# Kernel optimization log

Hardware: AMD Instinct MI355X
Metric: run time of the kernel (lower is better)

The kernel has to match this reference:

```python
import math
import jax, jax.numpy as jnp
import numpy as np

B, N_COLS, CHANNELS, NUM_HEADS = 512, 128, 512, 8
D_HEAD = CHANNELS // NUM_HEADS


def setup_inputs() -> dict:
    key = jax.random.key(0)
    ks = jax.random.split(key, 9)
    s = 1.0 / math.sqrt(CHANNELS)
    x = jax.random.normal(ks[0], (B, N_COLS, CHANNELS), dtype=jnp.float32)
    Wq = jax.random.uniform(ks[1], (CHANNELS, CHANNELS), jnp.float32, -s, s)
    bq = jax.random.uniform(ks[2], (CHANNELS,), jnp.float32, -s, s)
    Wk = jax.random.uniform(ks[3], (CHANNELS, CHANNELS), jnp.float32, -s, s)
    bk = jax.random.uniform(ks[4], (CHANNELS,), jnp.float32, -s, s)
    Wv = jax.random.uniform(ks[5], (CHANNELS, CHANNELS), jnp.float32, -s, s)
    bv = jax.random.uniform(ks[6], (CHANNELS,), jnp.float32, -s, s)
    Wo = jax.random.uniform(ks[7], (CHANNELS, CHANNELS), jnp.float32, -s, s)
    bo = jax.random.uniform(ks[8], (CHANNELS,), jnp.float32, -s, s)
    return {"x": x, "Wq": Wq, "bq": bq, "Wk": Wk, "bk": bk,
            "Wv": Wv, "bv": bv, "Wo": Wo, "bo": bo}


def reference(x, Wq, bq, Wk, bk, Wv, bv, Wo, bo):
    b, n, c = x.shape
    h, d = NUM_HEADS, D_HEAD

    def split_heads(t):  # [b, n, c] -> [b, h, n, d]
        return t.reshape(b, n, h, d).transpose(0, 2, 1, 3)

    Q = split_heads(x @ Wq + bq)
    K = split_heads(x @ Wk + bk)
    V = split_heads(x @ Wv + bv)

    # raw scores [b, h, q, k]
    scores = jnp.einsum('bhqd,bhkd->bhqk', Q, K)
    # causal mask over columns; note: mask added BEFORE scaling by sqrt(d)
    causal = jnp.tril(jnp.ones((n, n), dtype=jnp.float32))
    mask = (1.0 - causal) * -100000.0
    attn = jax.nn.softmax((scores + mask) / math.sqrt(d), axis=-1)
    out = jnp.einsum('bhqk,bhkd->bhqd', attn, V)
    out = out.transpose(0, 2, 1, 3).reshape(b, n, c)
    return out @ Wo + bo
```

## Files before the change

kernel.cpp:

```cpp
#include <hip/hip_runtime.h>

typedef _Float16 f16;
typedef _Float16 half8 __attribute__((ext_vector_type(8)));
typedef _Float16 half4 __attribute__((ext_vector_type(4)));
typedef float f32x4 __attribute__((ext_vector_type(4)));

#define B_SZ 512
#define NQ   128
#define CH   512
#define NH   8
#define DH   64
#define MTOK (B_SZ*NQ)
#define KD   512

#define MFMA16(a,b,c) __builtin_amdgcn_mfma_f32_16x16x32_f16((a),(b),(c),0,0,0)

#define GLDS16(g,l) __builtin_amdgcn_global_load_lds( \
    (__attribute__((address_space(1))) void*)(g), \
    (__attribute__((address_space(3))) void*)(l), 16, 0, 0)

__global__ __launch_bounds__(256) void k_cvt(const float* __restrict__ x,
                                             f16* __restrict__ xb) {
  const int n8 = MTOK * KD / 8;
  int i = blockIdx.x * blockDim.x + threadIdx.x;
  const int stride = gridDim.x * blockDim.x;
  for (; i < n8; i += stride) {
    f32x4 a = ((const f32x4*)x)[2 * i];
    f32x4 b = ((const f32x4*)x)[2 * i + 1];
    half8 h;
    h[0] = (f16)a[0]; h[1] = (f16)a[1]; h[2] = (f16)a[2]; h[3] = (f16)a[3];
    h[4] = (f16)b[0]; h[5] = (f16)b[1]; h[6] = (f16)b[2]; h[7] = (f16)b[3];
    ((half8*)xb)[i] = h;
  }
}

__global__ __launch_bounds__(256) void k_wt(const float* __restrict__ Wq,
                                            const float* __restrict__ Wk,
                                            const float* __restrict__ Wv,
                                            const float* __restrict__ Wo,
                                            f16* __restrict__ wt) {
  const int n = blockIdx.x;
  const float* W = (n < 512) ? Wq : (n < 1024) ? Wk : (n < 1536) ? Wv : Wo;
  const int c = n & 511;
  for (int k = threadIdx.x; k < 512; k += blockDim.x)
    wt[n * 512 + k] = (f16)W[k * 512 + c];
}


template<bool SW, int MB>
__device__ __forceinline__ void mfma16x(f32x4 (&acc)[8][4], half8 (&af)[4], half8 (&bf)[4]) {
#pragma unroll
  for (int i = 0; i < 4; ++i)
#pragma unroll
    for (int n = 0; n < 4; ++n) {
      if (SW) acc[MB + i][n] = MFMA16(bf[n], af[i], acc[MB + i][n]);
      else    acc[MB + i][n] = MFMA16(af[i], bf[n], acc[MB + i][n]);
    }
}

__device__ __forceinline__ void load4(const f16* base, half8 (&fr)[4]) {
#pragma unroll
  for (int n = 0; n < 4; ++n) fr[n] = *(const half8*)(base + n * 512);
}

#define BAR_MFMA_OPEN() __builtin_amdgcn_s_barrier(); \
  asm volatile("s_waitcnt lgkmcnt(0)" ::: "memory"); \
  __builtin_amdgcn_sched_barrier(0); \
  __builtin_amdgcn_s_setprio(1)
#define MFMA_CLOSE() __builtin_amdgcn_s_setprio(0); __builtin_amdgcn_s_barrier()
#define MFMA_CLOSE_GATE4() __builtin_amdgcn_s_setprio(0); \
  asm volatile("s_waitcnt vmcnt(4)" ::: "memory"); \
  __builtin_amdgcn_s_barrier()
#define MFMA_CLOSE_GATE0() __builtin_amdgcn_s_setprio(0); \
  asm volatile("s_waitcnt vmcnt(0)" ::: "memory"); \
  __builtin_amdgcn_s_barrier()

template<bool SW>
__device__ __forceinline__ void gemm256_main(
    const f16* __restrict__ Ag, const f16* __restrict__ Bg,
    int arow0, f16* lds, f32x4 (&acc)[8][4]) {
  const int tid = threadIdx.x;
  const int w = tid >> 6, lane = tid & 63;
  const int ln = lane & 15, g = lane >> 4;
  const int wm = w >> 2, wn = w & 3;
  const int slotx = ((g ^ ((ln >> 1) & 3)) << 3);

  f16* la = lds;
  f16* lb = lds + 32768;

  const int gsrc = (((tid & 3) ^ ((tid >> 3) & 3)) << 3);
  int soA[4], soB[4];
#pragma unroll
  for (int ks2 = 0; ks2 < 2; ++ks2)
#pragma unroll
    for (int r = 0; r < 2; ++r) {
      soA[ks2 * 2 + r] = (arow0 + r * 128 + (tid >> 2)) * KD + ks2 * 32 + gsrc;
      soB[ks2 * 2 + r] = (r * 128 + (tid >> 2)) * KD + ks2 * 32 + gsrc;
    }
  const int ldst = w * 512;

#define STAGE_A(t, ks2, r) GLDS16((f16*)Ag + soA[(ks2)*2+(r)] + (t)*64, \
      la + ((t)&1)*16384 + (ks2)*8192 + (r)*4096 + ldst)
#define STAGE_B(t, ks2, r) GLDS16((f16*)Bg + soB[(ks2)*2+(r)] + (t)*64, \
      lb + ((t)&1)*16384 + (ks2)*8192 + (r)*4096 + ldst)

  const int raA = (wm * 128 + ln) * 32 + slotx;
  const int raB = (wn * 64 + ln) * 32 + slotx;

  STAGE_A(0, 0, 0); STAGE_A(0, 0, 1); STAGE_B(0, 0, 0); STAGE_B(0, 0, 1);
  STAGE_A(0, 1, 0); STAGE_A(0, 1, 1); STAGE_B(0, 1, 0); STAGE_B(0, 1, 1);
  asm volatile("s_waitcnt vmcnt(0)" ::: "memory");
  __builtin_amdgcn_s_barrier();

  half8 af[4], bf[4];

#pragma unroll 1
  for (int t = 0; t < 7; ++t) {
    const int cur = t & 1;
    const f16* lac = la + cur * 16384;
    const f16* lbc = lb + cur * 16384;
    load4(lbc + raB, bf);
    load4(lac + raA, af);
    STAGE_A(t + 1, 0, 0); STAGE_A(t + 1, 0, 1);
    BAR_MFMA_OPEN(); mfma16x<SW, 0>(acc, af, bf); MFMA_CLOSE();
    load4(lac + raA + 4 * 512, af);
    STAGE_B(t + 1, 0, 0); STAGE_B(t + 1, 0, 1);
    BAR_MFMA_OPEN(); mfma16x<SW, 4>(acc, af, bf); MFMA_CLOSE_GATE4();
    load4(lbc + 8192 + raB, bf);
    load4(lac + 8192 + raA, af);
    STAGE_A(t + 1, 1, 0); STAGE_A(t + 1, 1, 1);
    BAR_MFMA_OPEN(); mfma16x<SW, 0>(acc, af, bf); MFMA_CLOSE();
    load4(lac + 8192 + raA + 4 * 512, af);
    STAGE_B(t + 1, 1, 0); STAGE_B(t + 1, 1, 1);
    BAR_MFMA_OPEN(); mfma16x<SW, 4>(acc, af, bf); MFMA_CLOSE_GATE4();
  }
  {
    const f16* lac = la + 16384;
    const f16* lbc = lb + 16384;
    load4(lbc + raB, bf);
    load4(lac + raA, af);
    BAR_MFMA_OPEN(); mfma16x<SW, 0>(acc, af, bf); MFMA_CLOSE();
    load4(lac + raA + 4 * 512, af);
    BAR_MFMA_OPEN(); mfma16x<SW, 4>(acc, af, bf); MFMA_CLOSE_GATE0();
    load4(lbc + 8192 + raB, bf);
    load4(lac + 8192 + raA, af);
    BAR_MFMA_OPEN(); mfma16x<SW, 0>(acc, af, bf); MFMA_CLOSE();
    load4(lac + 8192 + raA + 4 * 512, af);
    __builtin_amdgcn_s_barrier();
    asm volatile("s_waitcnt lgkmcnt(0)" ::: "memory");
    __builtin_amdgcn_sched_barrier(0);
    mfma16x<SW, 4>(acc, af, bf);
  }
#undef STAGE_A
#undef STAGE_B
}

__global__ __launch_bounds__(512, 2) void k_qk256(
    const f16* __restrict__ A, const f16* __restrict__ wt,
    const float* __restrict__ bq, const float* __restrict__ bk,
    f16* __restrict__ qb, f16* __restrict__ kb) {
  __shared__ f16 smem[65536];
  const int nwg8 = 1024 / 8;
  const int f = (blockIdx.x & 7) * nwg8 + (blockIdx.x >> 3);
  const int ntile = f & 3, mtile = f >> 2;
  const int arow0 = mtile * 256;
  const f16* Bg = wt + ntile * 256 * KD;

  f32x4 acc[8][4] = {};
  gemm256_main<true>(A, Bg, arow0, smem, acc);

  const int tid = threadIdx.x;
  const int w = tid >> 6, lane = tid & 63;
  const int ln = lane & 15, g = lane >> 4;
  const int wm = w >> 2, wn = w & 3;
  const int cslab = (ntile & 1) << 8;
  const float* bias = (ntile < 2) ? bq : bk;
  f16* dst = (ntile < 2) ? qb : kb;
#pragma unroll
  for (int n = 0; n < 4; ++n) {
    const int cg = cslab + wn * 64 + n * 16 + g * 4;
    const f32x4 b4 = *(const f32x4*)(bias + cg);
    const int h = cg >> 6, d = cg & 63;
#pragma unroll
    for (int m = 0; m < 8; ++m) {
      const int tk = arow0 + wm * 128 + m * 16 + ln;
      const int b = tk >> 7, tr = tk & 127;
      half4 o;
#pragma unroll
      for (int r = 0; r < 4; ++r) o[r] = (f16)(acc[m][n][r] + b4[r]);
      *(half4*)(dst + ((b * NH + h) * NQ + tr) * DH + d) = o;
    }
  }
}

__global__ __launch_bounds__(512, 2) void k_v256(
    const f16* __restrict__ A, const f16* __restrict__ wt,
    const float* __restrict__ bv, f16* __restrict__ vb) {
  __shared__ f16 smem[65536];
  const int nwg8 = 512 / 8;
  const int f = (blockIdx.x & 7) * nwg8 + (blockIdx.x >> 3);
  const int ntile = f & 1, mtile = f >> 1;
  const int arow0 = mtile * 256;
  const f16* Bg = wt + (1024 + ntile * 256) * KD;

  f32x4 acc[8][4] = {};
  gemm256_main<false>(A, Bg, arow0, smem, acc);

  const int tid = threadIdx.x;
  const int w = tid >> 6, lane = tid & 63;
  const int ln = lane & 15, g = lane >> 4;
  const int wm = w >> 2, wn = w & 3;
#pragma unroll
  for (int n = 0; n < 4; ++n) {
    const int cg = ntile * 256 + wn * 64 + n * 16 + ln;
    const float bias = bv[cg];
    const int h = cg >> 6, d = cg & 63;
#pragma unroll
    for (int m = 0; m < 8; ++m) {
      const int t0 = arow0 + wm * 128 + m * 16 + g * 4;
      const int b = t0 >> 7, tr = t0 & 127;
      half4 o;
#pragma unroll
      for (int r = 0; r < 4; ++r) o[r] = (f16)(acc[m][n][r] + bias);
      *(half4*)(vb + ((b * NH + h) * DH + d) * NQ + tr) = o;
    }
  }
}

__global__ __launch_bounds__(256, 2) void k_attn(
    const f16* __restrict__ qbuf, const f16* __restrict__ kbuf,
    const f16* __restrict__ vbuf, f16* __restrict__ ao) {
  __shared__ f16 kl[128 * 72];
  __shared__ f16 vl[64 * 136];
  __shared__ f16 pl[128 * 136];
  const int bh = blockIdx.x;
  const f16* Qp = qbuf + bh * (NQ * DH);
  const f16* Kp = kbuf + bh * (NQ * DH);
  const f16* Vp = vbuf + bh * (DH * NQ);
  const int tid = threadIdx.x;
  const int w = tid >> 6, lane = tid & 63;
  const int ln = lane & 15, g = lane >> 4;

#pragma unroll
  for (int i = 0; i < 4; ++i) {
    const int e = i * 2048 + tid * 8;
    *(half8*)(kl + (e >> 6) * 72 + (e & 63)) = *(const half8*)(Kp + e);
  }
#pragma unroll
  for (int i = 0; i < 4; ++i) {
    const int e = i * 2048 + tid * 8;
    *(half8*)(vl + (e >> 7) * 136 + (e & 127)) = *(const half8*)(Vp + e);
  }
  half8 qf[2][2];
#pragma unroll
  for (int m = 0; m < 2; ++m)
#pragma unroll
    for (int ks = 0; ks < 2; ++ks)
      qf[m][ks] = *(const half8*)(Qp + (w * 32 + m * 16 + ln) * DH + ks * 32 + g * 8);
  __syncthreads();

  f32x4 s[2][8] = {};
#pragma unroll
  for (int ks = 0; ks < 2; ++ks)
#pragma unroll
    for (int n = 0; n < 8; ++n) {
      half8 kf = *(const half8*)(kl + (n * 16 + ln) * 72 + ks * 32 + g * 8);
      s[0][n] = MFMA16(qf[0][ks], kf, s[0][n]);
      s[1][n] = MFMA16(qf[1][ks], kf, s[1][n]);
    }

  float inv[2][4];
#pragma unroll
  for (int m = 0; m < 2; ++m) {
#pragma unroll
    for (int r = 0; r < 4; ++r) {
      const int q = w * 32 + m * 16 + g * 4 + r;
      float z[8];
      float rm = -1e30f;
#pragma unroll
      for (int n = 0; n < 8; ++n) {
        const int col = n * 16 + ln;
        float zz = s[m][n][r] * 0.125f + ((col > q) ? -12500.0f : 0.0f);
        z[n] = zz;
        rm = fmaxf(rm, zz);
      }
      rm = fmaxf(rm, __shfl_xor(rm, 1));
      rm = fmaxf(rm, __shfl_xor(rm, 2));
      rm = fmaxf(rm, __shfl_xor(rm, 4));
      rm = fmaxf(rm, __shfl_xor(rm, 8));
      float rs = 0.f;
#pragma unroll
      for (int n = 0; n < 8; ++n) {
        const float p = __expf(z[n] - rm);
        rs += p;
        pl[q * 136 + n * 16 + ln] = (f16)p;
      }
      rs += __shfl_xor(rs, 1);
      rs += __shfl_xor(rs, 2);
      rs += __shfl_xor(rs, 4);
      rs += __shfl_xor(rs, 8);
      inv[m][r] = 1.0f / rs;
    }
  }

  f32x4 o[2][4] = {};
#pragma unroll
  for (int ks = 0; ks < 4; ++ks) {
    half8 pf0 = *(const half8*)(pl + (w * 32 + ln) * 136 + ks * 32 + g * 8);
    half8 pf1 = *(const half8*)(pl + (w * 32 + 16 + ln) * 136 + ks * 32 + g * 8);
#pragma unroll
    for (int n = 0; n < 4; ++n) {
      half8 vf = *(const half8*)(vl + (n * 16 + ln) * 136 + ks * 32 + g * 8);
      o[0][n] = MFMA16(pf0, vf, o[0][n]);
      o[1][n] = MFMA16(pf1, vf, o[1][n]);
    }
  }

  const int b = bh >> 3, h = bh & 7;
  f16* dst = ao + (b * NQ) * CH + h * DH;
#pragma unroll
  for (int m = 0; m < 2; ++m)
#pragma unroll
    for (int n = 0; n < 4; ++n)
#pragma unroll
      for (int r = 0; r < 4; ++r) {
        const int q = w * 32 + m * 16 + g * 4 + r;
        dst[q * CH + n * 16 + ln] = (f16)(o[m][n][r] * inv[m][r]);
      }
}

__global__ __launch_bounds__(512, 2) void k_out256(
    const f16* __restrict__ A, const f16* __restrict__ wt,
    const float* __restrict__ bo, float* __restrict__ out) {
  __shared__ f16 smem[65536];
  const int nwg8 = 512 / 8;
  const int f = (blockIdx.x & 7) * nwg8 + (blockIdx.x >> 3);
  const int ntile = f & 1, mtile = f >> 1;
  const int arow0 = mtile * 256;
  const f16* Bg = wt + (1536 + ntile * 256) * KD;

  f32x4 acc[8][4] = {};
  gemm256_main<true>(A, Bg, arow0, smem, acc);

  const int tid = threadIdx.x;
  const int w = tid >> 6, lane = tid & 63;
  const int ln = lane & 15, g = lane >> 4;
  const int wm = w >> 2, wn = w & 3;
#pragma unroll
  for (int n = 0; n < 4; ++n) {
    const int cg = ntile * 256 + wn * 64 + n * 16 + g * 4;
    const f32x4 b4 = *(const f32x4*)(bo + cg);
#pragma unroll
    for (int m = 0; m < 8; ++m) {
      const int tk = arow0 + wm * 128 + m * 16 + ln;
      f32x4 o = acc[m][n] + b4;
      *(f32x4*)(out + tk * CH + cg) = o;
    }
  }
}

extern "C" void kernel_launch(void* const* d_in, const int* in_sizes, int n_in,
                              void* d_out, int out_size, void* d_ws, size_t ws_size,
                              hipStream_t stream) {
  (void)in_sizes; (void)n_in; (void)out_size; (void)ws_size;
  const float* x  = (const float*)d_in[0];
  const float* Wq = (const float*)d_in[1];
  const float* bq = (const float*)d_in[2];
  const float* Wk = (const float*)d_in[3];
  const float* bk = (const float*)d_in[4];
  const float* Wv = (const float*)d_in[5];
  const float* bv = (const float*)d_in[6];
  const float* Wo = (const float*)d_in[7];
  const float* bo = (const float*)d_in[8];
  float* out = (float*)d_out;

  char* ws = (char*)d_ws;
  const size_t SZ = (size_t)MTOK * KD * sizeof(f16);
  f16* xb = (f16*)(ws);
  f16* qb = (f16*)(ws + SZ);
  f16* kb = (f16*)(ws + 2 * SZ);
  f16* vb = (f16*)(ws + 3 * SZ);
  f16* wt = (f16*)(ws + 4 * SZ);
  f16* ao = xb;

  k_cvt<<<2048, 256, 0, stream>>>(x, xb);
  k_wt<<<2048, 256, 0, stream>>>(Wq, Wk, Wv, Wo, wt);
  k_qk256<<<1024, 512, 0, stream>>>(xb, wt, bq, bk, qb, kb);
  k_v256<<<512, 512, 0, stream>>>(xb, wt, bv, vb);
  k_attn<<<4096, 256, 0, stream>>>(qb, kb, vb, ao);
  k_out256<<<512, 512, 0, stream>>>(ao, wt, bo, out);
}
```

Baseline: 330.0 us.

## Fuse attention with output projection in one per-batch kernel

Replaces the separate attention kernel and the output-projection GEMM with one kernel that handles one batch per block. It loops over the 8 heads, computes that head's attention output into LDS, then multiplies it by the matching slice of Wo, accumulating the projection in registers. This removes the round trip of the attention output through global memory and one kernel launch. In exchange, Wo fragments are read straight from global/L2 for every head and block with no LDS staging, there are only 512 blocks, each head step runs serially behind several barriers, and the large register accumulator may lower occupancy.

```diff
diff --git a/kernel.cpp b/kernel.cpp
--- a/kernel.cpp
+++ b/kernel.cpp
@@ -45,7 +45,6 @@
   for (int k = threadIdx.x; k < 512; k += blockDim.x)
     wt[n * 512 + k] = (f16)W[k * 512 + c];
 }
-
 
 template<bool SW, int MB>
 __device__ __forceinline__ void mfma16x(f32x4 (&acc)[8][4], half8 (&af)[4], half8 (&bf)[4]) {
@@ -227,62 +226,61 @@
   }
 }
 
-__global__ __launch_bounds__(256, 2) void k_attn(
+__global__ __launch_bounds__(512, 2) void k_fused(
     const f16* __restrict__ qbuf, const f16* __restrict__ kbuf,
-    const f16* __restrict__ vbuf, f16* __restrict__ ao) {
-  __shared__ f16 kl[128 * 72];
+    const f16* __restrict__ vbuf, const f16* __restrict__ wt,
+    const float* __restrict__ bo, float* __restrict__ out) {
+  __shared__ f16 klol[128 * 72];
   __shared__ f16 vl[64 * 136];
-  __shared__ f16 pl[128 * 136];
-  const int bh = blockIdx.x;
-  const f16* Qp = qbuf + bh * (NQ * DH);
-  const f16* Kp = kbuf + bh * (NQ * DH);
-  const f16* Vp = vbuf + bh * (DH * NQ);
+  __shared__ f16 pl[8 * 16 * 132];
+  const int b = blockIdx.x;
   const int tid = threadIdx.x;
   const int w = tid >> 6, lane = tid & 63;
   const int ln = lane & 15, g = lane >> 4;
-
-#pragma unroll
-  for (int i = 0; i < 4; ++i) {
-    const int e = i * 2048 + tid * 8;
-    *(half8*)(kl + (e >> 6) * 72 + (e & 63)) = *(const half8*)(Kp + e);
-  }
-#pragma unroll
-  for (int i = 0; i < 4; ++i) {
-    const int e = i * 2048 + tid * 8;
-    *(half8*)(vl + (e >> 7) * 136 + (e & 127)) = *(const half8*)(Vp + e);
-  }
-  half8 qf[2][2];
-#pragma unroll
-  for (int m = 0; m < 2; ++m)
-#pragma unroll
-    for (int ks = 0; ks < 2; ++ks)
-      qf[m][ks] = *(const half8*)(Qp + (w * 32 + m * 16 + ln) * DH + ks * 32 + g * 8);
-  __syncthreads();
-
-  f32x4 s[2][8] = {};
-#pragma unroll
-  for (int ks = 0; ks < 2; ++ks)
-#pragma unroll
-    for (int n = 0; n < 8; ++n) {
-      half8 kf = *(const half8*)(kl + (n * 16 + ln) * 72 + ks * 32 + g * 8);
-      s[0][n] = MFMA16(qf[0][ks], kf, s[0][n]);
-      s[1][n] = MFMA16(qf[1][ks], kf, s[1][n]);
-    }
-
-  float inv[2][4];
-#pragma unroll
-  for (int m = 0; m < 2; ++m) {
+  const int wm = w >> 2, wn = w & 3;
+  f16* plw = pl + w * (16 * 132);
+
+  f32x4 oacc[4][8] = {};
+
+#pragma unroll 1
+  for (int h = 0; h < 8; ++h) {
+    const f16* Kp = kbuf + (size_t)(b * NH + h) * (NQ * DH);
+    const f16* Vp = vbuf + (size_t)(b * NH + h) * (DH * NQ);
+    const f16* Qp = qbuf + (size_t)(b * NH + h) * (NQ * DH);
+#pragma unroll
+    for (int i = 0; i < 2; ++i) {
+      const int e = i * 4096 + tid * 8;
+      *(half8*)(klol + (e >> 6) * 72 + (e & 63)) = *(const half8*)(Kp + e);
+    }
+#pragma unroll
+    for (int i = 0; i < 2; ++i) {
+      const int e = i * 4096 + tid * 8;
+      *(half8*)(vl + (e >> 7) * 136 + (e & 127)) = *(const half8*)(Vp + e);
+    }
+    half8 qf[2];
+#pragma unroll
+    for (int kf = 0; kf < 2; ++kf)
+      qf[kf] = *(const half8*)(Qp + (w * 16 + ln) * DH + kf * 32 + g * 8);
+    __syncthreads();
+
+    f32x4 s[8] = {};
+#pragma unroll
+    for (int kf = 0; kf < 2; ++kf)
+#pragma unroll
+      for (int n = 0; n < 8; ++n) {
+        half8 kfr = *(const half8*)(klol + (n * 16 + ln) * 72 + kf * 32 + g * 8);
+        s[n] = MFMA16(qf[kf], kfr, s[n]);
+      }
+    float inv_[4];
 #pragma unroll
     for (int r = 0; r < 4; ++r) {
-      const int q = w * 32 + m * 16 + g * 4 + r;
-      float z[8];
-      float rm = -1e30f;
+      const int q = w * 16 + g * 4 + r;
+      float z[8], rm = -1e30f;
 #pragma unroll
       for (int n = 0; n < 8; ++n) {
         const int col = n * 16 + ln;
-        float zz = s[m][n][r] * 0.125f + ((col > q) ? -12500.0f : 0.0f);
-        z[n] = zz;
-        rm = fmaxf(rm, zz);
+        z[n] = s[n][r] * 0.125f + ((col > q) ? -12500.0f : 0.0f);
+        rm = fmaxf(rm, z[n]);
       }
       rm = fmaxf(rm, __shfl_xor(rm, 1));
       rm = fmaxf(rm, __shfl_xor(rm, 2));
@@ -293,68 +291,58 @@
       for (int n = 0; n < 8; ++n) {
         const float p = __expf(z[n] - rm);
         rs += p;
-        pl[q * 136 + n * 16 + ln] = (f16)p;
+        plw[(g * 4 + r) * 132 + n * 16 + ln] = (f16)p;
       }
       rs += __shfl_xor(rs, 1);
       rs += __shfl_xor(rs, 2);
       rs += __shfl_xor(rs, 4);
       rs += __shfl_xor(rs, 8);
-      inv[m][r] = 1.0f / rs;
-    }
-  }
-
-  f32x4 o[2][4] = {};
-#pragma unroll
-  for (int ks = 0; ks < 4; ++ks) {
-    half8 pf0 = *(const half8*)(pl + (w * 32 + ln) * 136 + ks * 32 + g * 8);
-    half8 pf1 = *(const half8*)(pl + (w * 32 + 16 + ln) * 136 + ks * 32 + g * 8);
-#pragma unroll
-    for (int n = 0; n < 4; ++n) {
-      half8 vf = *(const half8*)(vl + (n * 16 + ln) * 136 + ks * 32 + g * 8);
-      o[0][n] = MFMA16(pf0, vf, o[0][n]);
-      o[1][n] = MFMA16(pf1, vf, o[1][n]);
-    }
-  }
-
-  const int b = bh >> 3, h = bh & 7;
-  f16* dst = ao + (b * NQ) * CH + h * DH;
-#pragma unroll
-  for (int m = 0; m < 2; ++m)
+      inv_[r] = 1.0f / rs;
+    }
+    f32x4 o[4] = {};
+#pragma unroll
+    for (int kf = 0; kf < 4; ++kf) {
+      half8 pf = *(const half8*)(plw + ln * 132 + kf * 32 + g * 8);
+#pragma unroll
+      for (int n = 0; n < 4; ++n) {
+        half8 vf = *(const half8*)(vl + (n * 16 + ln) * 136 + kf * 32 + g * 8);
+        o[n] = MFMA16(pf, vf, o[n]);
+      }
+    }
+    __syncthreads();
 #pragma unroll
     for (int n = 0; n < 4; ++n)
 #pragma unroll
-      for (int r = 0; r < 4; ++r) {
-        const int q = w * 32 + m * 16 + g * 4 + r;
-        dst[q * CH + n * 16 + ln] = (f16)(o[m][n][r] * inv[m][r]);
-      }
-}
-
-__global__ __launch_bounds__(512, 2) void k_out256(
-    const f16* __restrict__ A, const f16* __restrict__ wt,
-    const float* __restrict__ bo, float* __restrict__ out) {
-  __shared__ f16 smem[65536];
-  const int nwg8 = 512 / 8;
-  const int f = (blockIdx.x & 7) * nwg8 + (blockIdx.x >> 3);
-  const int ntile = f & 1, mtile = f >> 1;
-  const int arow0 = mtile * 256;
-  const f16* Bg = wt + (1536 + ntile * 256) * KD;
-
-  f32x4 acc[8][4] = {};
-  gemm256_main<true>(A, Bg, arow0, smem, acc);
-
-  const int tid = threadIdx.x;
-  const int w = tid >> 6, lane = tid & 63;
-  const int ln = lane & 15, g = lane >> 4;
-  const int wm = w >> 2, wn = w & 3;
-#pragma unroll
-  for (int n = 0; n < 4; ++n) {
-    const int cg = ntile * 256 + wn * 64 + n * 16 + g * 4;
-    const f32x4 b4 = *(const f32x4*)(bo + cg);
-#pragma unroll
-    for (int m = 0; m < 8; ++m) {
-      const int tk = arow0 + wm * 128 + m * 16 + ln;
-      f32x4 o = acc[m][n] + b4;
-      *(f32x4*)(out + tk * CH + cg) = o;
+      for (int r = 0; r < 4; ++r)
+        klol[(w * 16 + g * 4 + r) * 72 + n * 16 + ln] = (f16)(o[n][r] * inv_[r]);
+    __syncthreads();
+    const f16* woh = wt + (size_t)(1536 + wn * 128) * KD + h * 64;
+    half8 of[4][2];
+#pragma unroll
+    for (int mt = 0; mt < 4; ++mt)
+#pragma unroll
+      for (int kf = 0; kf < 2; ++kf)
+        of[mt][kf] = *(const half8*)(klol + (wm * 64 + mt * 16 + ln) * 72 + kf * 32 + g * 8);
+#pragma unroll
+    for (int nt = 0; nt < 8; ++nt) {
+      half8 wf0 = *(const half8*)(woh + (nt * 16 + ln) * KD + g * 8);
+      half8 wf1 = *(const half8*)(woh + (nt * 16 + ln) * KD + 32 + g * 8);
+#pragma unroll
+      for (int mt = 0; mt < 4; ++mt) {
+        oacc[mt][nt] = MFMA16(wf0, of[mt][0], oacc[mt][nt]);
+        oacc[mt][nt] = MFMA16(wf1, of[mt][1], oacc[mt][nt]);
+      }
+    }
+    __syncthreads();
+  }
+#pragma unroll
+  for (int nt = 0; nt < 8; ++nt) {
+    const int chan = wn * 128 + nt * 16 + g * 4;
+    const f32x4 b4 = *(const f32x4*)(bo + chan);
+#pragma unroll
+    for (int mt = 0; mt < 4; ++mt) {
+      const int tok = b * NQ + wm * 64 + mt * 16 + ln;
+      *(f32x4*)(out + (size_t)tok * CH + chan) = oacc[mt][nt] + b4;
     }
   }
 }
@@ -381,12 +369,10 @@
   f16* kb = (f16*)(ws + 2 * SZ);
   f16* vb = (f16*)(ws + 3 * SZ);
   f16* wt = (f16*)(ws + 4 * SZ);
-  f16* ao = xb;
 
   k_cvt<<<2048, 256, 0, stream>>>(x, xb);
   k_wt<<<2048, 256, 0, stream>>>(Wq, Wk, Wv, Wo, wt);
   k_qk256<<<1024, 512, 0, stream>>>(xb, wt, bq, bk, qb, kb);
   k_v256<<<512, 512, 0, stream>>>(xb, wt, bv, vb);
-  k_attn<<<4096, 256, 0, stream>>>(qb, kb, vb, ao);
-  k_out256<<<512, 512, 0, stream>>>(ao, wt, bo, out);
-}
+  k_fused<<<512, 512, 0, stream>>>(qb, kb, vb, wt, bo, out);
+}
```

Measured after the change: 390.1 us. 1.18x slower.
